# Performance work log

Hardware: AMD Instinct MI355X
Metric: run time of the kernel (lower is better)

## Reference

```python
import jax, jax.numpy as jnp
import numpy as np

N_QUBITS = 8


def _rot_mats(p):
    # p: (n, 3) -> per-qubit 2x2 unitary RX(p2) @ RZ(p1) @ RY(p0), shape (n, 2, 2)
    a, b, c = 0.5 * p[:, 0], 0.5 * p[:, 1], 0.5 * p[:, 2]
    zc = jnp.zeros_like(a).astype(jnp.complex64)
    ca, sa = jnp.cos(a), jnp.sin(a)
    ry = jnp.stack([jnp.stack([ca, -sa], -1), jnp.stack([sa, ca], -1)], -2).astype(jnp.complex64)
    eb = jnp.exp(-1j * b)
    rz = jnp.stack([jnp.stack([eb, zc], -1), jnp.stack([zc, jnp.conj(eb)], -1)], -2)
    cc = jnp.cos(c).astype(jnp.complex64)
    sc = -1j * jnp.sin(c)
    rx = jnp.stack([jnp.stack([cc, sc], -1), jnp.stack([sc, cc], -1)], -2)
    return rx @ rz @ ry


def _qgate(x, params):
    # Batched statevector simulation of the PennyLane circuit.
    # x: (B, n) RX-encoding angles; params: (depth, n, 3). Wire 0 = most-significant bit.
    B, n = x.shape
    half = 0.5 * x
    # RX(x)|0> per qubit = [cos(x/2), -i sin(x/2)]
    amps = jnp.stack([jnp.cos(half).astype(jnp.complex64), (-1j) * jnp.sin(half)], axis=-1)  # (B,n,2)
    state = amps[:, 0]  # (B, 2)
    for q in range(1, n):
        state = (state[:, :, None] * amps[:, q][:, None, :]).reshape(B, -1)
    for d in range(params.shape[0]):
        U = _rot_mats(params[d])  # (n, 2, 2)
        for w in range(n):
            s = state.reshape(B, 2 ** w, 2, -1)
            s = jnp.einsum('ab,xlbr->xlar', U[w], s)
            state = s.reshape(B, -1)
        for c in range(n - 1):  # CNOT chain (c controls c+1)
            s = state.reshape(B, 2 ** c, 2, 2, -1)
            s = jnp.stack([s[:, :, 0], s[:, :, 1, ::-1]], axis=2)
            state = s.reshape(B, -1)
    probs = state.real ** 2 + state.imag ** 2  # (B, 2**n)
    k = np.arange(2 ** n)
    signs = (1.0 - 2.0 * (((k[None, :] >> (n - 1 - np.arange(n)[:, None])) & 1))).astype(np.float32)
    return probs @ jnp.asarray(signs).T  # (B, n) Pauli-Z expvals


def _apply_gate_list(x, params_list):
    # params_list: (n_gates, depth, n, 3); gates applied sequentially
    for g in range(params_list.shape[0]):
        x = _qgate(x, params_list[g])
    return x


def setup_inputs() -> dict:
    key = jax.random.key(0)
    ks = jax.random.split(key, 10)
    T, B, D, H, P, NQ, DP = 32, 64, 512, 512, 64, N_QUBITS, 2
    inputs = jax.random.normal(ks[0], (T, B, D), jnp.float32)
    W_proj = jax.random.normal(ks[1], (P, D + H), jnp.float32) / jnp.sqrt(jnp.float32(D + H))
    b_proj = jax.random.normal(ks[2], (P,), jnp.float32) * 0.01
    W_toq = jax.random.normal(ks[3], (NQ, P), jnp.float32) / jnp.sqrt(jnp.float32(P))
    W_q2h = jax.random.normal(ks[4], (H, NQ), jnp.float32) / jnp.sqrt(jnp.float32(NQ))
    f_params = jax.random.normal(ks[5], (DP, DP, NQ, 3), jnp.float32)
    i_params = jax.random.normal(ks[6], (DP, DP, NQ, 3), jnp.float32)
    g_params = jax.random.normal(ks[7], (DP, DP, NQ, 3), jnp.float32)
    o_params = jax.random.normal(ks[8], (DP, DP, NQ, 3), jnp.float32)
    return dict(inputs=inputs, W_proj=W_proj, b_proj=b_proj, W_toq=W_toq, W_q2h=W_q2h,
                f_params=f_params, i_params=i_params, g_params=g_params, o_params=o_params)


def reference(inputs, W_proj, b_proj, W_toq, W_q2h, f_params, i_params, g_params, o_params):
    B = inputs.shape[1]
    H = W_q2h.shape[0]

    def step(carry, x):
        hx, cx = carry
        combined = jnp.concatenate([x, hx], axis=1)          # (B, D+H)
        proj = combined @ W_proj.T + b_proj                   # (B, P)
        qin = proj @ W_toq.T                                  # (B, NQ)
        f = jax.nn.sigmoid(_apply_gate_list(qin, f_params) @ W_q2h.T)
        i = jax.nn.sigmoid(_apply_gate_list(qin, i_params) @ W_q2h.T)
        g = jnp.tanh(_apply_gate_list(qin, g_params) @ W_q2h.T)
        o = jax.nn.sigmoid(_apply_gate_list(qin, o_params) @ W_q2h.T)
        cx2 = f * cx + i * g
        hx2 = o * jnp.tanh(cx2)
        return (hx2, cx2), hx2

    init = (jnp.zeros((B, H), inputs.dtype), jnp.zeros((B, H), inputs.dtype))
    (hx, cx), stacked = jax.lax.scan(step, init, inputs)
    return stacked, hx, cx
```

## Files before the change

kernel.cpp:

```cpp
#include <hip/hip_runtime.h>
#include <math.h>

#define T_STEPS 32
#define BATCH 64

#define WS_WXQ 0
#define WS_WHQ 4096
#define WS_BQ  8192
#define WS_U   8208
#define WS_XQ  9232
#define WS_AB  25616

typedef float v2f __attribute__((ext_vector_type(2)));
typedef unsigned int u32x2 __attribute__((ext_vector_type(2)));
typedef __fp16 half4v __attribute__((ext_vector_type(4)));
typedef float f32x4 __attribute__((ext_vector_type(4)));

struct c32 { float x, y; };
__device__ __forceinline__ c32 cmul(c32 a, c32 b){ return {a.x*b.x - a.y*b.y, a.x*b.y + a.y*b.x}; }
__device__ __forceinline__ c32 cadd(c32 a, c32 b){ return {a.x+b.x, a.y+b.y}; }

__device__ __forceinline__ v2f mkv(float x, float y){ v2f r; r.x = x; r.y = y; return r; }
__device__ __forceinline__ v2f cmulv(v2f a, v2f b){
    return mkv(a.x, a.x) * b + mkv(-a.y, a.y) * mkv(b.y, b.x);
}
__device__ __forceinline__ float fast_sigmoid(float x){ return 1.f/(1.f + __expf(-x)); }
__device__ __forceinline__ float fast_tanh(float x){ float e = __expf(2.f*x); return 1.f - 2.f/(e+1.f); }

template<int C> __device__ __forceinline__ float dppf(float v){
    return __int_as_float(__builtin_amdgcn_mov_dpp(__float_as_int(v), C, 0xF, 0xF, true));
}
__device__ __forceinline__ float swap16(float v, int lane){
#if __has_builtin(__builtin_amdgcn_permlane16_swap)
    u32x2 r = __builtin_amdgcn_permlane16_swap(__float_as_uint(v), __float_as_uint(v), false, false);
    return __uint_as_float((lane & 16) ? r.x : r.y);
#else
    return __shfl_xor(v, 16);
#endif
}
__device__ __forceinline__ float swap32(float v, int lane){
#if __has_builtin(__builtin_amdgcn_permlane32_swap)
    u32x2 r = __builtin_amdgcn_permlane32_swap(__float_as_uint(v), __float_as_uint(v), false, false);
    return __uint_as_float((lane & 32) ? r.x : r.y);
#else
    return __shfl_xor(v, 32);
#endif
}
template<int LM> __device__ __forceinline__ float lanexor(float v, int lane){
    if constexpr (LM == 1)       return dppf<0xB1>(v);
    else if constexpr (LM == 2)  return dppf<0x4E>(v);
    else if constexpr (LM == 4)  return dppf<0x1B>(dppf<0x141>(v));
    else if constexpr (LM == 8)  return dppf<0x128>(v);
    else if constexpr (LM == 16) return swap16(v, lane);
    else                         return swap32(v, lane);
}
__device__ __forceinline__ float rdl(float v, int l){
    return __int_as_float(__builtin_amdgcn_readlane(__float_as_int(v), l));
}
__device__ __forceinline__ void fsincos(float rev, float* s, float* c){
#if __has_builtin(__builtin_amdgcn_sinf) && __has_builtin(__builtin_amdgcn_cosf)
    *s = __builtin_amdgcn_sinf(rev);
    *c = __builtin_amdgcn_cosf(rev);
#else
    __sincosf(rev * 6.2831853071795864f, s, c);
#endif
}

__device__ __forceinline__ void rot_u(const float* p3, float* dst){
    float a = 0.5f * p3[0], b = 0.5f * p3[1], c = 0.5f * p3[2];
    float ca = cosf(a), sa = sinf(a);
    float cb = cosf(b), sb = sinf(b);
    float cc = cosf(c), sc = sinf(c);
    c32 eb  = {cb, -sb};
    c32 ebc = {cb,  sb};
    c32 scx = {0.f, -sc};
    c32 m00 = { eb.x * ca,  eb.y * ca};
    c32 m01 = {-eb.x * sa, -eb.y * sa};
    c32 m10 = { ebc.x * sa, ebc.y * sa};
    c32 m11 = { ebc.x * ca, ebc.y * ca};
    c32 U00 = cadd(c32{cc * m00.x, cc * m00.y}, cmul(scx, m10));
    c32 U01 = cadd(c32{cc * m01.x, cc * m01.y}, cmul(scx, m11));
    c32 U10 = cadd(cmul(scx, m00), c32{cc * m10.x, cc * m10.y});
    c32 U11 = cadd(cmul(scx, m01), c32{cc * m11.x, cc * m11.y});
    dst[0] = U00.x; dst[1] = U00.y; dst[2] = U01.x; dst[3] = U01.y;
    dst[4] = U10.x; dst[5] = U10.y; dst[6] = U11.x; dst[7] = U11.y;
}

__global__ void precompute_kernel(const float* __restrict__ W_proj,
                                  const float* __restrict__ b_proj,
                                  const float* __restrict__ W_toq,
                                  const float* __restrict__ fP, const float* __restrict__ iP,
                                  const float* __restrict__ gP, const float* __restrict__ oP,
                                  float* __restrict__ ws)
{
    int tid = threadIdx.x;
    int blk = blockIdx.x;
    if (blk < 32) {
        int idx = blk * 256 + tid;
        int q = idx >> 10, dd = idx & 1023;
        float acc = 0.f;
        for (int p = 0; p < 64; ++p) acc += W_toq[q * 64 + p] * W_proj[p * 1024 + dd];
        if (dd < 512) ws[WS_WXQ + q * 512 + dd] = acc;
        else          ws[WS_WHQ + q * 512 + (dd - 512)] = acc;
        if (idx < 8) {
            float a2 = 0.f;
            for (int p = 0; p < 64; ++p) a2 += W_toq[idx * 64 + p] * b_proj[p];
            ws[WS_BQ + idx] = a2;
        }
    } else if (blk == 32) {
        if (tid < 128) {
            int gt = tid >> 5, rest = tid & 31;
            const float* P = (gt == 0) ? fP : (gt == 1) ? iP : (gt == 2) ? gP : oP;
            int g = (rest >> 4) & 1, d = (rest >> 3) & 1, w = rest & 7;
            rot_u(P + (((g * 2 + d) * 8 + w) * 3), ws + WS_U + tid * 8);
        }
    } else {
        __shared__ float sW[8][8];
        int combo = blk - 33;
        int gt = combo >> 1, gl = combo & 1;
        if (tid < 8) {
            const float* P = (gt == 0) ? fP : (gt == 1) ? iP : (gt == 2) ? gP : oP;
            rot_u(P + (((gl * 2 + 1) * 8 + tid) * 3), &sW[tid][0]);
        }
        __syncthreads();
        int rp = tid >> 4, rr = tid & 15;
        c32 pa = {1.f, 0.f};
        #pragma unroll
        for (int w = 0; w < 4; ++w) {
            int i = (rp >> (3 - w)) & 1, j = (rr >> (3 - w)) & 1;
            c32 e = {sW[w][(i * 2 + j) * 2], sW[w][(i * 2 + j) * 2 + 1]};
            pa = cmul(pa, e);
        }
        ws[WS_AB + combo * 1024 + tid * 2]     = pa.x;
        ws[WS_AB + combo * 1024 + tid * 2 + 1] = pa.y;
        c32 pb = {1.f, 0.f};
        #pragma unroll
        for (int w = 4; w < 8; ++w) {
            int i = (rp >> (7 - w)) & 1, j = (rr >> (7 - w)) & 1;
            c32 e = {sW[w][(i * 2 + j) * 2], sW[w][(i * 2 + j) * 2 + 1]};
            pb = cmul(pb, e);
        }
        ws[WS_AB + combo * 1024 + 512 + tid * 2]     = pb.x;
        ws[WS_AB + combo * 1024 + 512 + tid * 2 + 1] = pb.y;
    }
}

__global__ void xq_kernel(const float* __restrict__ inputs, float* __restrict__ ws)
{
    __shared__ float xs[512];
    int row = blockIdx.x;
    int tid = threadIdx.x;
    xs[tid]       = inputs[row * 512 + tid];
    xs[tid + 256] = inputs[row * 512 + 256 + tid];
    __syncthreads();
    int g = tid >> 5, j = tid & 31;
    const float* w = ws + WS_WXQ + g * 512;
    float acc = 0.f;
    #pragma unroll 4
    for (int i = 0; i < 16; ++i) acc += xs[j + 32 * i] * w[j + 32 * i];
    acc += __shfl_xor(acc, 1);  acc += __shfl_xor(acc, 2);
    acc += __shfl_xor(acc, 4);  acc += __shfl_xor(acc, 8);
    acc += __shfl_xor(acc, 16);
    if (j == 0) ws[WS_XQ + row * 8 + g] = acc + ws[WS_BQ + g];
}

__global__ __launch_bounds__(256, 1)
void recurrence_kernel(const float* __restrict__ W_q2h,
                       const float* __restrict__ ws,
                       float* __restrict__ out)
{
    __shared__ __align__(16) float sU[1024];
    __shared__ __align__(16) float sXq[T_STEPS * 8];
    __shared__ __align__(16) float sexpW[4][8];
    __shared__ __align__(16) float qpartW[4][8];
    __shared__ __align__(16) float sH[T_STEPS * 512];

    int tid = threadIdx.x;
    int b   = blockIdx.x;
    int wv  = tid >> 6;
    int lane = tid & 63;
    int l = lane;

    for (int i = tid; i < 1024; i += 256) sU[i] = ws[WS_U + i];
    sXq[tid] = ws[WS_XQ + ((tid >> 3) * 64 + b) * 8 + (tid & 7)];
    if (tid < 32) ((float*)qpartW)[tid] = 0.f;

    v2f wha2[4], whb2[4];
    #pragma unroll
    for (int j = 0; j < 4; ++j) {
        wha2[j] = mkv(ws[WS_WHQ + (2*j) * 512 + tid],       ws[WS_WHQ + (2*j+1) * 512 + tid]);
        whb2[j] = mkv(ws[WS_WHQ + (2*j) * 512 + tid + 256], ws[WS_WHQ + (2*j+1) * 512 + tid + 256]);
    }
    v2f w2hp[8];
    {
        float4 a0 = *(const float4*)&W_q2h[tid * 8];
        float4 a1 = *(const float4*)&W_q2h[tid * 8 + 4];
        float4 b0 = *(const float4*)&W_q2h[(tid + 256) * 8];
        float4 b1 = *(const float4*)&W_q2h[(tid + 256) * 8 + 4];
        w2hp[0] = mkv(a0.x, b0.x); w2hp[1] = mkv(a0.y, b0.y);
        w2hp[2] = mkv(a0.z, b0.z); w2hp[3] = mkv(a0.w, b0.w);
        w2hp[4] = mkv(a1.x, b1.x); w2hp[5] = mkv(a1.y, b1.y);
        w2hp[6] = mkv(a1.z, b1.z); w2hp[7] = mkv(a1.w, b1.w);
    }

    half4v ArT[2], AiT[2], nAiT[2], Brf[2], Bif[2], nBif[2];
    {
        int q4 = lane >> 4, n = lane & 15;
        #pragma unroll
        for (int gl = 0; gl < 2; ++gl) {
            const float* Ab = ws + WS_AB + (wv * 2 + gl) * 1024;
            const float* Bb = Ab + 512;
            #pragma unroll
            for (int j = 0; j < 4; ++j) {
                int k = 4 * q4 + j;
                float ar = Ab[(n * 16 + k) * 2], ai = Ab[(n * 16 + k) * 2 + 1];
                float br = Bb[(n * 16 + k) * 2], bi = Bb[(n * 16 + k) * 2 + 1];
                ArT[gl][j]  = (__fp16)ar;  AiT[gl][j] = (__fp16)ai;  nAiT[gl][j] = (__fp16)(-ai);
                Brf[gl][j]  = (__fp16)br;  Bif[gl][j] = (__fp16)bi;  nBif[gl][j] = (__fp16)(-bi);
            }
        }
    }

    __syncthreads();

    v2f sA0[2], sB0[2], sA1[2], sB1[2], sA5[2], sB5[2], sA6[2], sB6[2], sA7[2], sB7[2];
    v2f A2a[2], B2a[2], A2b[2], B2b[2];
    v2f A3a[2], B3a[2], A3b[2], B3b[2];
    v2f A4a[2], B4a[2], A4b[2], B4b[2];
    {
        int s0 = (l >> 5) & 1;
        int s1 = ((l >> 5) ^ (l >> 4)) & 1;
        int s5 = ((l >> 3) ^ (l >> 2)) & 1;
        int s6 = ((l >> 2) ^ (l >> 1)) & 1;
        int s7 = ((l >> 1) ^ l) & 1;
        int L4 = (l >> 4) & 1;
        int L3 = (l >> 3) & 1;
        #pragma unroll
        for (int gl = 0; gl < 2; ++gl) {
            const float* d0 = sU + (wv * 32 + gl * 16) * 8;
            auto colA = [&](int q, int c){ const float* m = d0 + q * 8 + c * 4; return mkv(m[0], m[1]); };
            auto colB = [&](int q, int c){ const float* m = d0 + q * 8 + c * 4; return mkv(m[3 - c * 4 + c * 4 + 3 - 3 + 3], 0.f); };
            #define CA(q,c) mkv(d0[(q)*8 + (c)*4 + 0], d0[(q)*8 + (c)*4 + 1])
            #define CB(q,c) mkv(d0[(q)*8 + (c)*4 + 3], -d0[(q)*8 + (c)*4 + 2])
            sA0[gl] = s0 ? CA(0,1) : CA(0,0);  sB0[gl] = s0 ? CB(0,1) : CB(0,0);
            sA1[gl] = s1 ? CA(1,1) : CA(1,0);  sB1[gl] = s1 ? CB(1,1) : CB(1,0);
            sA5[gl] = s5 ? CA(5,1) : CA(5,0);  sB5[gl] = s5 ? CB(5,1) : CB(5,0);
            sA6[gl] = s6 ? CA(6,1) : CA(6,0);  sB6[gl] = s6 ? CB(6,1) : CB(6,0);
            sA7[gl] = s7 ? CA(7,1) : CA(7,0);  sB7[gl] = s7 ? CB(7,1) : CB(7,0);
            A2a[gl] = L4 ? CA(2,1) : CA(2,0);  B2a[gl] = L4 ? CB(2,1) : CB(2,0);
            A2b[gl] = L4 ? CA(2,0) : CA(2,1);  B2b[gl] = L4 ? CB(2,0) : CB(2,1);
            A3a[gl] = CA(3,0);                 B3a[gl] = CB(3,0);
            A3b[gl] = CA(3,1);                 B3b[gl] = CB(3,1);
            A4a[gl] = L3 ? CA(4,1) : CA(4,0);  B4a[gl] = L3 ? CB(4,1) : CB(4,0);
            A4b[gl] = L3 ? CA(4,0) : CA(4,1);  B4b[gl] = L3 ? CB(4,0) : CB(4,1);
            #undef CA
            #undef CB
            (void)colA; (void)colB;
        }
    }
    float sg[6];
    #pragma unroll
    for (int st = 0; st < 6; ++st) sg[st] = ((l >> st) & 1) ? -1.f : 1.f;

    const float REVC = 0.07957747154594767f;
    const f32x4 zacc = {0.f, 0.f, 0.f, 0.f};
    float c0 = 0.f, c1 = 0.f, h0 = 0.f, h1 = 0.f;

    for (int t = 0; t < T_STEPS; ++t) {
        float ang[8];
        {
            const v2f* qw = (const v2f*)qpartW;
            const v2f* xq2 = (const v2f*)&sXq[t * 8];
            #pragma unroll
            for (int j = 0; j < 4; ++j) {
                v2f s_ = ((qw[j] + qw[4 + j]) + (qw[8 + j] + qw[12 + j]) + xq2[j]) * REVC;
                ang[2 * j] = s_.x; ang[2 * j + 1] = s_.y;
            }
        }

        float e[8];
        #pragma unroll
        for (int gl = 0; gl < 2; ++gl) {
            float sh[8], ch[8];
            #pragma unroll
            for (int q = 0; q < 8; ++q) fsincos(ang[q], &sh[q], &ch[q]);

            v2f u0 = ch[0] * sA0[gl] + sh[0] * sB0[gl];
            v2f u1 = ch[1] * sA1[gl] + sh[1] * sB1[gl];
            v2f u5 = ch[5] * sA5[gl] + sh[5] * sB5[gl];
            v2f u6 = ch[6] * sA6[gl] + sh[6] * sB6[gl];
            v2f u7 = ch[7] * sA7[gl] + sh[7] * sB7[gl];
            v2f u2a = ch[2] * A2a[gl] + sh[2] * B2a[gl];
            v2f u2b = ch[2] * A2b[gl] + sh[2] * B2b[gl];
            v2f u3a = ch[3] * A3a[gl] + sh[3] * B3a[gl];
            v2f u3b = ch[3] * A3b[gl] + sh[3] * B3b[gl];
            v2f u4a = ch[4] * A4a[gl] + sh[4] * B4a[gl];
            v2f u4b = ch[4] * A4b[gl] + sh[4] * B4b[gl];

            v2f hi = cmulv(u0, u1);
            v2f lo = cmulv(cmulv(u5, u6), u7);
            v2f hilo = cmulv(hi, lo);
            v2f u23_0 = cmulv(u2a, u3a);
            v2f u23_1 = cmulv(u2a, u3b);
            v2f u23_2 = cmulv(u2b, u3b);
            v2f u23_3 = cmulv(u2b, u3a);
            v2f mid0 = cmulv(u23_0, u4a);
            v2f mid1 = cmulv(u23_1, u4b);
            v2f mid2 = cmulv(u23_2, u4a);
            v2f mid3 = cmulv(u23_3, u4b);
            v2f a0 = cmulv(hilo, mid0);
            v2f a1 = cmulv(hilo, mid1);
            v2f a2 = cmulv(hilo, mid2);
            v2f a3 = cmulv(hilo, mid3);

            half4v Sr, Si;
            Sr[0] = (__fp16)a0.x; Sr[1] = (__fp16)a1.x; Sr[2] = (__fp16)a2.x; Sr[3] = (__fp16)a3.x;
            Si[0] = (__fp16)a0.y; Si[1] = (__fp16)a1.y; Si[2] = (__fp16)a2.y; Si[3] = (__fp16)a3.y;

            f32x4 TrT = __builtin_amdgcn_mfma_f32_16x16x16f16(Sr, ArT[gl], zacc, 0, 0, 0);
            TrT = __builtin_amdgcn_mfma_f32_16x16x16f16(Si, nAiT[gl], TrT, 0, 0, 0);
            f32x4 TiT = __builtin_amdgcn_mfma_f32_16x16x16f16(Sr, AiT[gl], zacc, 0, 0, 0);
            TiT = __builtin_amdgcn_mfma_f32_16x16x16f16(Si, ArT[gl], TiT, 0, 0, 0);
            half4v TrH, TiH;
            #pragma unroll
            for (int j = 0; j < 4; ++j) { TrH[j] = (__fp16)TrT[j]; TiH[j] = (__fp16)TiT[j]; }
            f32x4 Xr = __builtin_amdgcn_mfma_f32_16x16x16f16(Brf[gl], TrH, zacc, 0, 0, 0);
            Xr = __builtin_amdgcn_mfma_f32_16x16x16f16(nBif[gl], TiH, Xr, 0, 0, 0);
            f32x4 Xi = __builtin_amdgcn_mfma_f32_16x16x16f16(Brf[gl], TiH, zacc, 0, 0, 0);
            Xi = __builtin_amdgcn_mfma_f32_16x16x16f16(Bif[gl], TrH, Xi, 0, 0, 0);

            float p0 = Xr[0]*Xr[0] + Xi[0]*Xi[0];
            float p1 = Xr[1]*Xr[1] + Xi[1]*Xi[1];
            float p2 = Xr[2]*Xr[2] + Xi[2]*Xi[2];
            float p3 = Xr[3]*Xr[3] + Xi[3]*Xi[3];
            float w0v = (p0 + p1) + (p2 + p3);
            float w6v = (p0 + p1) - (p2 + p3);
            float w7v = (p0 - p1) - (p2 - p3);
            #define WHT_STAGE(LM, ST) { float v_; \
                v_ = lanexor<LM>(w0v, lane); w0v = __builtin_fmaf(sg[ST], w0v, v_); \
                v_ = lanexor<LM>(w6v, lane); w6v = __builtin_fmaf(sg[ST], w6v, v_); \
                v_ = lanexor<LM>(w7v, lane); w7v = __builtin_fmaf(sg[ST], w7v, v_); }
            WHT_STAGE(1, 0) WHT_STAGE(2, 1) WHT_STAGE(4, 2)
            WHT_STAGE(8, 3) WHT_STAGE(16, 4) WHT_STAGE(32, 5)
            #undef WHT_STAGE
            e[0] = rdl(w0v, 8);  e[1] = rdl(w0v, 12); e[2] = rdl(w0v, 14);
            e[3] = rdl(w0v, 15); e[4] = rdl(w0v, 47); e[5] = rdl(w0v, 63);
            e[6] = rdl(w6v, 63); e[7] = rdl(w7v, 63);
            if (gl == 0) {
                #pragma unroll
                for (int q = 0; q < 8; ++q) ang[q] = e[q] * REVC;
            }
        }
        if (lane == 0) {
            float4 e0v; e0v.x = e[0]; e0v.y = e[1]; e0v.z = e[2]; e0v.w = e[3];
            float4 e1v; e1v.x = e[4]; e1v.y = e[5]; e1v.z = e[6]; e1v.w = e[7];
            *(float4*)&sexpW[wv][0] = e0v;
            *(float4*)&sexpW[wv][4] = e1v;
        }
        __syncthreads();

        {
            v2f pre[4];
            #pragma unroll
            for (int g = 0; g < 4; ++g) {
                float4 ea = *(const float4*)&sexpW[g][0];
                float4 eb2 = *(const float4*)&sexpW[g][4];
                v2f acc = ea.x * w2hp[0] + ea.y * w2hp[1] + ea.z * w2hp[2] + ea.w * w2hp[3]
                        + eb2.x * w2hp[4] + eb2.y * w2hp[5] + eb2.z * w2hp[6] + eb2.w * w2hp[7];
                pre[g] = acc;
            }
            float f0 = fast_sigmoid(pre[0].x), i0 = fast_sigmoid(pre[1].x);
            float g0 = fast_tanh(pre[2].x),    o0 = fast_sigmoid(pre[3].x);
            c0 = f0 * c0 + i0 * g0;  h0 = o0 * fast_tanh(c0);
            float f1 = fast_sigmoid(pre[0].y), i1 = fast_sigmoid(pre[1].y);
            float g1 = fast_tanh(pre[2].y),    o1 = fast_sigmoid(pre[3].y);
            c1 = f1 * c1 + i1 * g1;  h1 = o1 * fast_tanh(c1);
            sH[t * 512 + tid]       = h0;
            sH[t * 512 + tid + 256] = h1;
        }

        {
            v2f pp[4];
            #pragma unroll
            for (int j = 0; j < 4; ++j) pp[j] = wha2[j] * h0 + whb2[j] * h1;
            #pragma unroll
            for (int j = 0; j < 4; ++j) {
                pp[j] += mkv(lanexor<1>(pp[j].x, lane), lanexor<1>(pp[j].y, lane));
                pp[j] += mkv(lanexor<2>(pp[j].x, lane), lanexor<2>(pp[j].y, lane));
                pp[j] += mkv(lanexor<4>(pp[j].x, lane), lanexor<4>(pp[j].y, lane));
            }
            int sel = lane & 7;
            float y = (sel == 0) ? pp[0].x : (sel == 1) ? pp[0].y
                    : (sel == 2) ? pp[1].x : (sel == 3) ? pp[1].y
                    : (sel == 4) ? pp[2].x : (sel == 5) ? pp[2].y
                    : (sel == 6) ? pp[3].x : pp[3].y;
            y += lanexor<8>(y, lane);
            y += swap16(y, lane);
            y += swap32(y, lane);
            if (lane < 8) qpartW[wv][lane] = y;
        }
        __syncthreads();
    }

    {
        const float4* src = (const float4*)sH;
        float4* dst = (float4*)out;
        #pragma unroll
        for (int k = 0; k < 16; ++k) {
            int i = k * 256 + tid;
            int t = i >> 7, h4 = i & 127;
            dst[(t * 64 + b) * 128 + h4] = src[i];
        }
    }
    float* hx_out = out + (size_t)T_STEPS * 64 * 512;
    float* cx_out = hx_out + 64 * 512;
    hx_out[b * 512 + tid]       = h0;
    hx_out[b * 512 + tid + 256] = h1;
    cx_out[b * 512 + tid]       = c0;
    cx_out[b * 512 + tid + 256] = c1;
}

extern "C" void kernel_launch(void* const* d_in, const int* in_sizes, int n_in,
                              void* d_out, int out_size, void* d_ws, size_t ws_size,
                              hipStream_t stream)
{
    const float* inputs = (const float*)d_in[0];
    const float* W_proj = (const float*)d_in[1];
    const float* b_proj = (const float*)d_in[2];
    const float* W_toq  = (const float*)d_in[3];
    const float* W_q2h  = (const float*)d_in[4];
    const float* fP     = (const float*)d_in[5];
    const float* iP     = (const float*)d_in[6];
    const float* gP     = (const float*)d_in[7];
    const float* oP     = (const float*)d_in[8];
    float* ws  = (float*)d_ws;
    float* out = (float*)d_out;

    precompute_kernel<<<41, 256, 0, stream>>>(W_proj, b_proj, W_toq, fP, iP, gP, oP, ws);
    xq_kernel<<<T_STEPS * BATCH, 256, 0, stream>>>(inputs, ws);
    recurrence_kernel<<<BATCH, 256, 0, stream>>>(W_q2h, ws, out);
}
```

Measured before the change: 150.5 us.

## Fuse input-to-qubit projection into recurrence kernel, dropping separate xq launch

Removes the standalone xq_kernel and computes each batch row's input projection inside the recurrence kernel. Each block stages its 32 time steps of inputs into the sH shared buffer and the 8x512 projection weights into a new shared array, then each thread computes one (t, qubit) dot product. This drops one kernel launch and the global round trip for the projected values. In exchange, only 64 blocks now do all the input reads and the 512-long serial dot products, and shared memory use grows by 16KB.

Result: slower. 156.1 us (+3.7%).

```diff
diff --git a/kernel.cpp b/kernel.cpp
--- a/kernel.cpp
+++ b/kernel.cpp
@@ -8,7 +8,6 @@
 #define WS_WHQ 4096
 #define WS_BQ  8192
 #define WS_U   8208
-#define WS_XQ  9232
 #define WS_AB  25616
 
 typedef float v2f __attribute__((ext_vector_type(2)));
@@ -145,31 +144,14 @@
     }
 }
 
-__global__ void xq_kernel(const float* __restrict__ inputs, float* __restrict__ ws)
-{
-    __shared__ float xs[512];
-    int row = blockIdx.x;
-    int tid = threadIdx.x;
-    xs[tid]       = inputs[row * 512 + tid];
-    xs[tid + 256] = inputs[row * 512 + 256 + tid];
-    __syncthreads();
-    int g = tid >> 5, j = tid & 31;
-    const float* w = ws + WS_WXQ + g * 512;
-    float acc = 0.f;
-    #pragma unroll 4
-    for (int i = 0; i < 16; ++i) acc += xs[j + 32 * i] * w[j + 32 * i];
-    acc += __shfl_xor(acc, 1);  acc += __shfl_xor(acc, 2);
-    acc += __shfl_xor(acc, 4);  acc += __shfl_xor(acc, 8);
-    acc += __shfl_xor(acc, 16);
-    if (j == 0) ws[WS_XQ + row * 8 + g] = acc + ws[WS_BQ + g];
-}
-
 __global__ __launch_bounds__(256, 1)
-void recurrence_kernel(const float* __restrict__ W_q2h,
+void recurrence_kernel(const float* __restrict__ inputs,
+                       const float* __restrict__ W_q2h,
                        const float* __restrict__ ws,
                        float* __restrict__ out)
 {
     __shared__ __align__(16) float sU[1024];
+    __shared__ __align__(16) float sWxq[4096];
     __shared__ __align__(16) float sXq[T_STEPS * 8];
     __shared__ __align__(16) float sexpW[4][8];
     __shared__ __align__(16) float qpartW[4][8];
@@ -181,8 +163,21 @@
     int lane = tid & 63;
     int l = lane;
 
+    {
+        const float4* gin = (const float4*)inputs;
+        float4* s4 = (float4*)sH;
+        #pragma unroll
+        for (int kk = 0; kk < 16; ++kk) {
+            int i = kk * 256 + tid;
+            int t = i >> 7, c = i & 127;
+            s4[t * 128 + c] = gin[(t * 64 + b) * 128 + c];
+        }
+        const float4* gw = (const float4*)(ws + WS_WXQ);
+        float4* w4 = (float4*)sWxq;
+        #pragma unroll
+        for (int kk = 0; kk < 4; ++kk) w4[kk * 256 + tid] = gw[kk * 256 + tid];
+    }
     for (int i = tid; i < 1024; i += 256) sU[i] = ws[WS_U + i];
-    sXq[tid] = ws[WS_XQ + ((tid >> 3) * 64 + b) * 8 + (tid & 7)];
     if (tid < 32) ((float*)qpartW)[tid] = 0.f;
 
     v2f wha2[4], whb2[4];
@@ -223,6 +218,20 @@
 
     __syncthreads();
 
+    {
+        int tq = tid;
+        int t = tq >> 3, q = tq & 7;
+        const float4* xr = (const float4*)(sH + t * 512);
+        const float4* wr = (const float4*)(sWxq + q * 512);
+        float acc = 0.f;
+        #pragma unroll 8
+        for (int k = 0; k < 128; ++k) {
+            float4 a = xr[k], w = wr[k];
+            acc += a.x * w.x + a.y * w.y + a.z * w.z + a.w * w.w;
+        }
+        sXq[tq] = acc + ws[WS_BQ + q];
+    }
+
     v2f sA0[2], sB0[2], sA1[2], sB1[2], sA5[2], sB5[2], sA6[2], sB6[2], sA7[2], sB7[2];
     v2f A2a[2], B2a[2], A2b[2], B2b[2];
     v2f A3a[2], B3a[2], A3b[2], B3b[2];
@@ -238,8 +247,6 @@
         #pragma unroll
         for (int gl = 0; gl < 2; ++gl) {
             const float* d0 = sU + (wv * 32 + gl * 16) * 8;
-            auto colA = [&](int q, int c){ const float* m = d0 + q * 8 + c * 4; return mkv(m[0], m[1]); };
-            auto colB = [&](int q, int c){ const float* m = d0 + q * 8 + c * 4; return mkv(m[3 - c * 4 + c * 4 + 3 - 3 + 3], 0.f); };
             #define CA(q,c) mkv(d0[(q)*8 + (c)*4 + 0], d0[(q)*8 + (c)*4 + 1])
             #define CB(q,c) mkv(d0[(q)*8 + (c)*4 + 3], -d0[(q)*8 + (c)*4 + 2])
             sA0[gl] = s0 ? CA(0,1) : CA(0,0);  sB0[gl] = s0 ? CB(0,1) : CB(0,0);
@@ -255,7 +262,6 @@
             A4b[gl] = L3 ? CA(4,0) : CA(4,1);  B4b[gl] = L3 ? CB(4,0) : CB(4,1);
             #undef CA
             #undef CB
-            (void)colA; (void)colB;
         }
     }
     float sg[6];
@@ -265,6 +271,8 @@
     const float REVC = 0.07957747154594767f;
     const f32x4 zacc = {0.f, 0.f, 0.f, 0.f};
     float c0 = 0.f, c1 = 0.f, h0 = 0.f, h1 = 0.f;
+
+    __syncthreads();
 
     for (int t = 0; t < T_STEPS; ++t) {
         float ang[8];
@@ -437,6 +445,5 @@
     float* out = (float*)d_out;
 
     precompute_kernel<<<41, 256, 0, stream>>>(W_proj, b_proj, W_toq, fP, iP, gP, oP, ws);
-    xq_kernel<<<T_STEPS * BATCH, 256, 0, stream>>>(inputs, ws);
-    recurrence_kernel<<<BATCH, 256, 0, stream>>>(W_q2h, ws, out);
-}
+    recurrence_kernel<<<BATCH, 256, 0, stream>>>(inputs, W_q2h, ws, out);
+}
```
